# Kernel optimization log

Hardware: AMD Instinct MI355X
Metric: run time of the kernel (lower is better)

## Reference

```python
import jax, jax.numpy as jnp
import numpy as np

B, N, N2 = 4, 4096, 4096
CIN, DIM, KNN, UP = 128, 64, 20, 2
HPOS, HATT = 64, 256
EPS = 1e-5


def _group(feat, idx):
    # feat: (B,C,M), idx: (B,N,K) -> (B,C,N,K) gather of neighbor features
    return jax.vmap(lambda f, i: f[:, i])(feat, idx)


def _conv1d(w, b, x):
    # 1x1 Conv1d: w (O,C), x (B,C,N)
    return jnp.einsum('oc,bcn->bon', w, x) + b[:, None]


def _bn(x, g, be, m, v):
    # eval-mode BatchNorm2d on (B,C,N,K)
    inv = g / jnp.sqrt(v + EPS)
    return x * inv[:, None, None] + (be - m * inv)[:, None, None]


def setup_inputs() -> dict:
    key = jax.random.key(0)
    ks = jax.random.split(key, 32)
    r = lambda i, s: jax.random.normal(ks[i], s, jnp.float32)
    u = lambda i, s: jax.random.uniform(ks[i], s, jnp.float32, 0.5, 1.5)
    return {
        'pos1': r(0, (B, 3, N)),
        'query': r(1, (B, CIN, N)),
        'pos2': r(2, (B, 3, N2)),
        'key_feat': r(3, (B, CIN, N2)),
        'wq': r(4, (DIM, CIN)) * 0.05, 'bq': r(5, (DIM,)) * 0.05,
        'wk': r(6, (DIM, CIN)) * 0.05, 'bk': r(7, (DIM,)) * 0.05,
        'wv': r(8, (DIM, CIN)) * 0.05, 'bv': r(9, (DIM,)) * 0.05,
        'pw1': r(10, (HPOS, 3)) * 0.2, 'pb1': r(11, (HPOS,)) * 0.05,
        'pg': u(12, (HPOS,)), 'pbt': r(13, (HPOS,)) * 0.05,
        'pm': r(14, (HPOS,)) * 0.05, 'pv': u(15, (HPOS,)),
        'pw2': r(16, (DIM, HPOS)) * 0.1, 'pb2': r(17, (DIM,)) * 0.05,
        'aw1': r(18, (HATT, DIM)) * 0.1, 'ab1': r(19, (HATT,)) * 0.05,
        'ag': u(20, (HATT,)), 'abt2': r(21, (HATT,)) * 0.05,
        'am': r(22, (HATT,)) * 0.05, 'av': u(23, (HATT,)),
        'awt': r(24, (HATT, DIM, UP)) * 0.05, 'abt': r(25, (DIM,)) * 0.05,
        'we': r(26, (CIN, DIM)) * 0.1, 'be': r(27, (CIN,)) * 0.05,
    }


def reference(pos1, query, pos2, key_feat, wq, bq, wk, bk, wv, bv,
              pw1, pb1, pg, pbt, pm, pv, pw2, pb2,
              aw1, ab1, ag, abt2, am, av, awt, abt, we, be):
    q = _conv1d(wq, bq, query)          # (B,DIM,N)
    k = _conv1d(wk, bk, key_feat)       # (B,DIM,N2)
    v = _conv1d(wv, bv, key_feat)       # (B,DIM,N2)
    # KNN of pos1 queries into pos2 support set
    p1 = pos1.transpose(0, 2, 1)        # (B,N,3)
    p2 = pos2.transpose(0, 2, 1)        # (B,N2,3)
    d = (jnp.sum(p1 * p1, -1)[:, :, None] + jnp.sum(p2 * p2, -1)[:, None, :]
         - 2.0 * jnp.einsum('bnd,bmd->bnm', p1, p2))
    _, idx = jax.lax.top_k(-d, KNN)     # (B,N,KNN)
    kg = _group(k, idx)                 # (B,DIM,N,K)
    qk_rel = q[:, :, :, None] - kg
    pos_rel = pos1[:, :, :, None] - _group(pos2, idx)   # (B,3,N,K)
    # pos_mlp: conv2d 3->HPOS, BN, ReLU, conv2d HPOS->DIM
    pe = jnp.einsum('oc,bcnk->bonk', pw1, pos_rel) + pb1[:, None, None]
    pe = jax.nn.relu(_bn(pe, pg, pbt, pm, pv))
    pe = jnp.einsum('oc,bcnk->bonk', pw2, pe) + pb2[:, None, None]  # (B,DIM,N,K)
    # attn_mlp: conv2d DIM->HATT, BN, ReLU, ConvTranspose2d HATT->DIM kernel (UP,1)
    h = qk_rel + pe
    a = jnp.einsum('oc,bcnk->bonk', aw1, h) + ab1[:, None, None]
    a = jax.nn.relu(_bn(a, ag, abt2, am, av))               # (B,HATT,N,K)
    att = jnp.einsum('bcnk,cor->bonrk', a, awt).reshape(B, DIM, N * UP, KNN)
    att = att + abt[:, None, None]
    att = jax.nn.softmax(att, axis=-1)
    vg = _group(v, idx) + pe            # (B,DIM,N,K)
    vu = jnp.repeat(vg, UP, axis=2)     # nearest upsample -> (B,DIM,N*UP,K)
    agg = jnp.sum(att * vu, axis=-1)    # (B,DIM,N*UP)
    y = _conv1d(we, be, agg)            # (B,CIN,N*UP)
    identity = jnp.repeat(query, UP, axis=2)  # residual (in==out -> Identity)
    return y + identity
```

## Files before the change

kernel.cpp:

```cpp
#include <hip/hip_runtime.h>
#include <hip/hip_bf16.h>

#define BATCH 4
#define NPTS  4096
#define NPTS2 4096
#define CIN   128
#define DIM   64
#define KNN   20
#define UPF   2
#define HPOS  64
#define HATT  256
#define MOUT  8192
#define EPSF  1e-5f
#define QPB   3
#define BPB   1366

typedef _Float16 h16x8 __attribute__((ext_vector_type(8)));
typedef _Float16 h16x4 __attribute__((ext_vector_type(4)));
typedef _Float16 h16x2 __attribute__((ext_vector_type(2)));
typedef float    f32x4 __attribute__((ext_vector_type(4)));

__device__ inline float rdlane(float v, int src) {
  return __int_as_float(__builtin_amdgcn_readlane(__float_as_int(v), src));
}

__device__ __forceinline__ float distf(float qn, float m2x, float m2y, float m2z,
                                       float x, float y, float z) {
  float s = __fmaf_rn(x, x, qn);
  s = __fmaf_rn(y, y, s);
  s = __fmaf_rn(z, z, s);
  s = __fmaf_rn(m2x, x, s);
  s = __fmaf_rn(m2y, y, s);
  s = __fmaf_rn(m2z, z, s);
  return s;
}

__global__ __launch_bounds__(256) void proj_q(const float* __restrict__ x,
    const float* __restrict__ wq, const float* __restrict__ bq,
    float* __restrict__ q_t) {
  __shared__ float X[CIN][64];
  __shared__ float O[64][65];
  const int b  = blockIdx.x >> 6;
  const int n0 = (blockIdx.x & 63) * 64;
  const int t  = threadIdx.x;
  for (int l = t; l < CIN * 64; l += 256) {
    int c = l >> 6, i = l & 63;
    X[c][i] = x[(b * CIN + c) * NPTS + n0 + i];
  }
  __syncthreads();
  const int n_l = t & 63;
  const int w   = __builtin_amdgcn_readfirstlane(t >> 6);
  float acc[16];
#pragma unroll
  for (int i = 0; i < 16; ++i) acc[i] = bq[w * 16 + i];
  for (int c = 0; c < CIN; ++c) {
    float xv = X[c][n_l];
#pragma unroll
    for (int i = 0; i < 16; ++i) acc[i] += wq[(w * 16 + i) * CIN + c] * xv;
  }
#pragma unroll
  for (int i = 0; i < 16; ++i) O[n_l][w * 16 + i] = acc[i];
  __syncthreads();
  for (int l = t; l < 64 * 64; l += 256)
    q_t[(b * NPTS + n0 + (l >> 6)) * DIM + (l & 63)] = O[l >> 6][l & 63];
}

__global__ __launch_bounds__(256) void proj_kv(const float* __restrict__ x,
    const float* __restrict__ wk, const float* __restrict__ bk,
    const float* __restrict__ wv, const float* __restrict__ bv,
    float* __restrict__ k_t, float* __restrict__ v_t) {
  __shared__ float X[CIN][64];
  __shared__ float O[64][65];
  const int b  = blockIdx.x >> 6;
  const int n0 = (blockIdx.x & 63) * 64;
  const int t  = threadIdx.x;
  for (int l = t; l < CIN * 64; l += 256) {
    int c = l >> 6, i = l & 63;
    X[c][i] = x[(b * CIN + c) * NPTS2 + n0 + i];
  }
  __syncthreads();
  const int n_l = t & 63;
  const int w   = __builtin_amdgcn_readfirstlane(t >> 6);
  float acck[16], accv[16];
#pragma unroll
  for (int i = 0; i < 16; ++i) { acck[i] = bk[w * 16 + i]; accv[i] = bv[w * 16 + i]; }
  for (int c = 0; c < CIN; ++c) {
    float xv = X[c][n_l];
#pragma unroll
    for (int i = 0; i < 16; ++i) {
      acck[i] += wk[(w * 16 + i) * CIN + c] * xv;
      accv[i] += wv[(w * 16 + i) * CIN + c] * xv;
    }
  }
#pragma unroll
  for (int i = 0; i < 16; ++i) O[n_l][w * 16 + i] = acck[i];
  __syncthreads();
  for (int l = t; l < 64 * 64; l += 256)
    k_t[(b * NPTS2 + n0 + (l >> 6)) * DIM + (l & 63)] = O[l >> 6][l & 63];
  __syncthreads();
#pragma unroll
  for (int i = 0; i < 16; ++i) O[n_l][w * 16 + i] = accv[i];
  __syncthreads();
  for (int l = t; l < 64 * 64; l += 256)
    v_t[(b * NPTS2 + n0 + (l >> 6)) * DIM + (l & 63)] = O[l >> 6][l & 63];
}

__global__ __launch_bounds__(256) void knn_kernel(const float* __restrict__ pos1,
    const float* __restrict__ pos2, int* __restrict__ idxout) {
  __shared__ int   cntS[16];
  __shared__ float dbufS[16][64];
  __shared__ int   jbufS[16][64];
  const int lane = threadIdx.x & 63;
  const int wv   = threadIdx.x >> 6;
  const int b    = blockIdx.x >> 8;
  const int nb   = (blockIdx.x & 255) * 16;
  const float* p2x = pos2 + (b * 3 + 0) * NPTS2;
  const float* p2y = pos2 + (b * 3 + 1) * NPTS2;
  const float* p2z = pos2 + (b * 3 + 2) * NPTS2;

  float qn[4], m2x[4], m2y[4], m2z[4];
#pragma unroll
  for (int qi = 0; qi < 4; ++qi) {
    int n = nb + wv * 4 + qi;
    float qx = pos1[(b * 3 + 0) * NPTS + n];
    float qy = pos1[(b * 3 + 1) * NPTS + n];
    float qz = pos1[(b * 3 + 2) * NPTS + n];
    qn[qi]  = qx * qx + qy * qy + qz * qz;
    m2x[qi] = -2.0f * qx; m2y[qi] = -2.0f * qy; m2z[qi] = -2.0f * qz;
  }

  float mymin[4] = {3.402823466e38f, 3.402823466e38f,
                    3.402823466e38f, 3.402823466e38f};
  f32x4 cx[4], cy[4], cz[4];
#pragma unroll 1
  for (int c = 0; c < 4; ++c) {
    int base = c * 1024 + lane * 4;
#pragma unroll
    for (int g = 0; g < 4; ++g) {
      cx[g] = *(const f32x4*)(p2x + base + g * 256);
      cy[g] = *(const f32x4*)(p2y + base + g * 256);
      cz[g] = *(const f32x4*)(p2z + base + g * 256);
    }
#pragma unroll
    for (int qi = 0; qi < 4; ++qi)
#pragma unroll
      for (int g = 0; g < 4; ++g)
#pragma unroll
        for (int e = 0; e < 4; ++e) {
          float d = distf(qn[qi], m2x[qi], m2y[qi], m2z[qi],
                          cx[g][e], cy[g][e], cz[g][e]);
          mymin[qi] = fminf(mymin[qi], d);
        }
  }

  float T0[4];
#pragma unroll
  for (int qi = 0; qi < 4; ++qi) {
    float v = mymin[qi];
#pragma unroll
    for (int k = 2; k <= 64; k <<= 1)
#pragma unroll
      for (int jj = k >> 1; jj >= 1; jj >>= 1) {
        float o = __shfl_xor(v, jj);
        bool up = ((lane & k) == 0);
        bool keepmin = (((lane & jj) == 0) == up);
        v = keepmin ? fminf(v, o) : fmaxf(v, o);
      }
    T0[qi] = rdlane(v, 19);
  }

  if (lane < 4) cntS[wv * 4 + lane] = 0;

#pragma unroll 1
  for (int c = 0; c < 4; ++c) {
    int base = c * 1024 + lane * 4;
#pragma unroll
    for (int g = 0; g < 4; ++g) {
      cx[g] = *(const f32x4*)(p2x + base + g * 256);
      cy[g] = *(const f32x4*)(p2y + base + g * 256);
      cz[g] = *(const f32x4*)(p2z + base + g * 256);
    }
#pragma unroll
    for (int qi = 0; qi < 4; ++qi) {
      const int qq = wv * 4 + qi;
#pragma unroll
      for (int g = 0; g < 4; ++g)
#pragma unroll
        for (int e = 0; e < 4; ++e) {
          float d = distf(qn[qi], m2x[qi], m2y[qi], m2z[qi],
                          cx[g][e], cy[g][e], cz[g][e]);
          if (d <= T0[qi]) {
            int slot = atomicAdd(&cntS[qq], 1);
            if (slot < 64) { dbufS[qq][slot] = d; jbufS[qq][slot] = base + g * 256 + e; }
          }
        }
    }
  }

#pragma unroll 1
  for (int qi = 0; qi < 4; ++qi) {
    const int qq = wv * 4 + qi;
    const int n  = nb + qq;
    const int cnt = cntS[qq];
    if (cnt <= 64) {
      float dk = (lane < cnt) ? dbufS[qq][lane] : 3.402823466e38f;
      int   jk = (lane < cnt) ? jbufS[qq][lane] : 0x7fffffff;
#pragma unroll
      for (int k = 2; k <= 64; k <<= 1) {
#pragma unroll
        for (int jj = k >> 1; jj >= 1; jj >>= 1) {
          float od = __shfl_xor(dk, jj);
          int   oj = __shfl_xor(jk, jj);
          bool mineSm = (dk < od) || (dk == od && jk < oj);
          bool up = ((lane & k) == 0);
          bool keepmin = (((lane & jj) == 0) == up);
          bool takeOther = (keepmin != mineSm);
          dk = takeOther ? od : dk;
          jk = takeOther ? oj : jk;
        }
      }
      if (lane < KNN) idxout[(b * NPTS + n) * KNN + lane] = jk;
    } else {
      float dl = 3.402823466e38f;
      int   il = 0;
      for (int j0 = 0; j0 < NPTS2; j0 += 64) {
        int j = j0 + lane;
        float d = distf(qn[qi], m2x[qi], m2y[qi], m2z[qi], p2x[j], p2y[j], p2z[j]);
        float T = rdlane(dl, 19);
        unsigned long long m = __ballot(d < T);
        while (m) {
          int src = __ffsll(m) - 1;
          m &= m - 1;
          float dd = rdlane(d, src);
          float T2 = rdlane(dl, 19);
          if (dd < T2) {
            int jj2 = j0 + src;
            float pd = __shfl_up(dl, 1);
            int   pi = __shfl_up(il, 1);
            if (dl > dd) {
              if (lane == 0 || pd <= dd) { dl = dd; il = jj2; }
              else                       { dl = pd; il = pi; }
            }
          }
        }
      }
      if (lane < KNN) idxout[(b * NPTS + n) * KNN + lane] = il;
    }
  }
}

__global__ __launch_bounds__(256) void pack_weights(
    const float* __restrict__ aw1, const float* __restrict__ awt,
    const float* __restrict__ pw2,
    const float* __restrict__ ag,  const float* __restrict__ av,
    const float* __restrict__ abt2, const float* __restrict__ am,
    const float* __restrict__ abt,
    const float* __restrict__ pg,  const float* __restrict__ pv,
    const float* __restrict__ pbt, const float* __restrict__ pm,
    const float* __restrict__ ab1, const float* __restrict__ pb1,
    const float* __restrict__ pw1,
    _Float16* __restrict__ aw1h, _Float16* __restrict__ awtP,
    _Float16* __restrict__ pw2h, float* __restrict__ abtX,
    float* __restrict__ ab1f, float* __restrict__ pw1f,
    float* __restrict__ pb1f) {
  int i = blockIdx.x * 256 + threadIdx.x;
  if (i < 16384) {
    int j = i >> 6;
    float inv = ag[j] / sqrtf(av[j] + EPSF);
    aw1h[i] = (_Float16)(aw1[i] * inv);
  }
  if (i < 32768) {
    int orr = i >> 8, j = i & 255;
    awtP[i] = (_Float16)awt[j * 128 + orr];
  }
  if (i < 4096) pw2h[i] = (_Float16)pw2[i];
  if (i < 256) {
    float inv = ag[i] / sqrtf(av[i] + EPSF);
    ab1f[i] = ab1[i] * inv + (abt2[i] - am[i] * inv);
  }
  if (i < 192) {
    int hc = i / 3;
    float inv = pg[hc] / sqrtf(pv[hc] + EPSF);
    pw1f[i] = pw1[i] * inv;
  }
  if (i < 128) abtX[i] = abt[i >> 1];
  if (i < 64) {
    float inv = pg[i] / sqrtf(pv[i] + EPSF);
    pb1f[i] = pb1[i] * inv + (pbt[i] - pm[i] * inv);
  }
}

#define SM_R0    0
#define SM_R1    9216
#define SM_LGC   0
#define SM_VGB   18432

__global__ __launch_bounds__(256, 4) void attn_mfma(
    const float* __restrict__ q_t, const float* __restrict__ k_t,
    const float* __restrict__ v_t, const int* __restrict__ idx,
    const float* __restrict__ pos1, const float* __restrict__ pos2,
    const float* __restrict__ pw1f, const float* __restrict__ pb1f,
    const _Float16* __restrict__ pw2h, const float* __restrict__ pb2,
    const _Float16* __restrict__ aw1h, const float* __restrict__ ab1f,
    const _Float16* __restrict__ awtP, const float* __restrict__ abtX,
    float* __restrict__ agg) {
  __shared__ __align__(16) char smem[27136];
  const int b  = blockIdx.x / BPB;
  const int n0 = (blockIdx.x - b * BPB) * QPB;
  const int t  = threadIdx.x;
  const int lane = t & 63;
  const int w  = t >> 6;
  const int r  = lane & 15;
  const int q4 = lane >> 4;

  const int colB = t & 63, cgB = t >> 6;
  const int pB = colB / 20, kkB = colB - pB * 20;
  const bool okB = (pB < QPB) && (n0 + pB < NPTS);
  const int nqB = okB ? (n0 + pB) : 0;
  int jB = 0;
  if (okB) jB = idx[(b * NPTS + nqB) * KNN + kkB];

  f32x4 qk4[4], vv4[4];
  {
    const float* qrow = q_t + ((size_t)(b * NPTS  + nqB)) * DIM + cgB * 16;
    const float* krow = k_t + ((size_t)(b * NPTS2 + jB))  * DIM + cgB * 16;
    const float* vrow = v_t + ((size_t)(b * NPTS2 + jB))  * DIM + cgB * 16;
#pragma unroll
    for (int u = 0; u < 4; ++u) {
      f32x4 qv = *(const f32x4*)(qrow + u * 4);
      f32x4 kv = *(const f32x4*)(krow + u * 4);
      qk4[u] = qv - kv;
      vv4[u] = *(const f32x4*)(vrow + u * 4);
    }
  }

  {
    float p0 = 0.f, p1 = 0.f, p2 = 0.f;
    if (okB) {
      p0 = pos1[(b * 3 + 0) * NPTS + nqB] - pos2[(b * 3 + 0) * NPTS2 + jB];
      p1 = pos1[(b * 3 + 1) * NPTS + nqB] - pos2[(b * 3 + 1) * NPTS2 + jB];
      p2 = pos1[(b * 3 + 2) * NPTS + nqB] - pos2[(b * 3 + 2) * NPTS2 + jB];
    }
#pragma unroll
    for (int hf = 0; hf < 2; ++hf) {
      h16x8 pk;
#pragma unroll
      for (int ii = 0; ii < 8; ++ii) {
        int hc = cgB * 16 + hf * 8 + ii;
        float v0 = pb1f[hc] + pw1f[hc*3] * p0 + pw1f[hc*3+1] * p1 + pw1f[hc*3+2] * p2;
        v0 = fmaxf(v0, 0.f);
        if (!okB) v0 = 0.f;
        pk[ii] = (_Float16)v0;
      }
      *(h16x8*)(smem + SM_R0 + ((colB * 72 + cgB * 16 + hf * 8) * 2)) = pk;
    }
  }
  __syncthreads();

  {
    h16x8 a0[2];
#pragma unroll
    for (int ks = 0; ks < 2; ++ks)
      a0[ks] = *(const h16x8*)&pw2h[(w * 16 + r) * 64 + ks * 32 + q4 * 8];
    f32x4 acc[4];
#pragma unroll
    for (int nt = 0; nt < 4; ++nt) acc[nt] = (f32x4){0.f, 0.f, 0.f, 0.f};
#pragma unroll
    for (int ks = 0; ks < 2; ++ks)
#pragma unroll
      for (int nt = 0; nt < 4; ++nt) {
        h16x8 bv = *(h16x8*)(smem + SM_R0 + ((nt * 16 + r) * 72 + ks * 32 + q4 * 8) * 2);
        acc[nt] = __builtin_amdgcn_mfma_f32_16x16x32_f16(a0[ks], bv, acc[nt], 0, 0, 0);
      }
    int o0 = w * 16 + q4 * 4;
    f32x4 pbv = *(const f32x4*)&pb2[o0];
#pragma unroll
    for (int nt = 0; nt < 4; ++nt) {
      f32x4 vv = acc[nt] + pbv;
      h16x4 pk = {(_Float16)vv[0], (_Float16)vv[1], (_Float16)vv[2], (_Float16)vv[3]};
      *(h16x4*)(smem + SM_R1 + ((nt * 16 + r) * 72 + o0) * 2) = pk;
    }
  }

  {
    h16x8 pe8[2];
#pragma unroll
    for (int hf = 0; hf < 2; ++hf)
      pe8[hf] = *(h16x8*)(smem + SM_R1 + (colB * 72 + cgB * 16 + hf * 8) * 2);
    h16x8 hp8[2];
#pragma unroll
    for (int u = 0; u < 4; ++u) {
      int hf = u >> 1, e0 = (u & 1) * 4;
      f32x4 pe = {(float)pe8[hf][e0],     (float)pe8[hf][e0 + 1],
                  (float)pe8[hf][e0 + 2], (float)pe8[hf][e0 + 3]};
      f32x4 hv = qk4[u] + pe;
      f32x4 gv = vv4[u] + pe;
      if (!okB) { hv = (f32x4){0.f,0.f,0.f,0.f}; gv = hv; }
      hp8[hf][e0]     = (_Float16)hv[0];
      hp8[hf][e0 + 1] = (_Float16)hv[1];
      hp8[hf][e0 + 2] = (_Float16)hv[2];
      hp8[hf][e0 + 3] = (_Float16)hv[3];
      h16x4 gp = {(_Float16)gv[0], (_Float16)gv[1], (_Float16)gv[2], (_Float16)gv[3]};
      *(h16x4*)(smem + SM_VGB + (colB * 68 + cgB * 16 + u * 4) * 2) = gp;
    }
#pragma unroll
    for (int hf = 0; hf < 2; ++hf)
      *(h16x8*)(smem + SM_R1 + (colB * 72 + cgB * 16 + hf * 8) * 2) = hp8[hf];
  }
  __syncthreads();

  h16x8 bs[2][4];
#pragma unroll
  for (int ks = 0; ks < 2; ++ks)
#pragma unroll
    for (int nt = 0; nt < 4; ++nt)
      bs[ks][nt] = *(h16x8*)(smem + SM_R1 + ((nt * 16 + r) * 72 + ks * 32 + q4 * 8) * 2);

  f32x4 accD[2][4];
#pragma unroll
  for (int h = 0; h < 2; ++h)
#pragma unroll
    for (int nt = 0; nt < 4; ++nt) accD[h][nt] = (f32x4){0.f, 0.f, 0.f, 0.f};

#define C_QUARTER(quar, base)                                                  \
  {                                                                            \
    int mt = (quar) * 4 + w;                                                   \
    h16x8 af0 = *(const h16x8*)&aw1h[(mt * 16 + r) * 64 + q4 * 8];             \
    h16x8 af1 = *(const h16x8*)&aw1h[(mt * 16 + r) * 64 + 32 + q4 * 8];        \
    f32x4 acc[4];                                                              \
    _Pragma("unroll")                                                          \
    for (int nt = 0; nt < 4; ++nt) acc[nt] = (f32x4){0.f, 0.f, 0.f, 0.f};      \
    _Pragma("unroll")                                                          \
    for (int nt = 0; nt < 4; ++nt)                                             \
      acc[nt] = __builtin_amdgcn_mfma_f32_16x16x32_f16(af0, bs[0][nt], acc[nt], 0, 0, 0); \
    _Pragma("unroll")                                                          \
    for (int nt = 0; nt < 4; ++nt)                                             \
      acc[nt] = __builtin_amdgcn_mfma_f32_16x16x32_f16(af1, bs[1][nt], acc[nt], 0, 0, 0); \
    int j0  = mt * 16 + q4 * 4;                                                \
    int jq0 = j0 - (quar) * 64;                                                \
    f32x4 b1 = *(const f32x4*)&ab1f[j0];                                       \
    _Pragma("unroll")                                                          \
    for (int nt = 0; nt < 4; ++nt) {                                           \
      int col = nt * 16 + r;                                                   \
      float v0 = fmaxf(acc[nt][0] + b1[0], 0.f);                               \
      float v1 = fmaxf(acc[nt][1] + b1[1], 0.f);                               \
      float v2 = fmaxf(acc[nt][2] + b1[2], 0.f);                               \
      float v3 = fmaxf(acc[nt][3] + b1[3], 0.f);                               \
      h16x4 pk = {(_Float16)v0, (_Float16)v1, (_Float16)v2, (_Float16)v3};     \
      *(h16x4*)(smem + (base) + (col * 72 + jq0) * 2) = pk;                    \
    }                                                                          \
  }

#define D_QUARTER(quar, base)                                                  \
  {                                                                            \
    _Pragma("unroll")                                                          \
    for (int ks2 = 0; ks2 < 2; ++ks2) {                                        \
      h16x8 bsv[4];                                                            \
      _Pragma("unroll")                                                        \
      for (int nt = 0; nt < 4; ++nt)                                           \
        bsv[nt] = *(h16x8*)(smem + (base) + ((nt * 16 + r) * 72 + ks2 * 32 + q4 * 8) * 2); \
      int ksg = (quar) * 2 + ks2;                                              \
      _Pragma("unroll")                                                        \
      for (int h = 0; h < 2; ++h) {                                            \
        int mt2 = w * 2 + h;                                                   \
        h16x8 af = *(const h16x8*)&awtP[(mt2 * 16 + r) * 256 + ksg * 32 + q4 * 8]; \
        _Pragma("unroll")                                                      \
        for (int nt = 0; nt < 4; ++nt)                                         \
          accD[h][nt] = __builtin_amdgcn_mfma_f32_16x16x32_f16(af, bsv[nt], accD[h][nt], 0, 0, 0); \
      }                                                                        \
    }                                                                          \
  }

  C_QUARTER(0, SM_R0)
  __syncthreads();
  D_QUARTER(0, SM_R0)
  C_QUARTER(1, SM_R1)
  __syncthreads();
  D_QUARTER(1, SM_R1)
  C_QUARTER(2, SM_R0)
  __syncthreads();
  D_QUARTER(2, SM_R0)
  C_QUARTER(3, SM_R1)
  __syncthreads();
  D_QUARTER(3, SM_R1)
  __syncthreads();

  {
#pragma unroll
    for (int h = 0; h < 2; ++h) {
      int orr0 = (w * 2 + h) * 16 + q4 * 4;
      f32x4 ab = *(const f32x4*)&abtX[orr0];
#pragma unroll
      for (int nt = 0; nt < 4; ++nt) {
        int col = nt * 16 + r;
        if (col < QPB * KNN) {
          f32x4 vv = accD[h][nt] + ab;
          h16x4 pk = {(_Float16)vv[0], (_Float16)vv[1], (_Float16)vv[2], (_Float16)vv[3]};
          *(h16x4*)(smem + SM_LGC + (col * 136 + orr0) * 2) = pk;
        }
      }
    }
  }
  __syncthreads();

  if (t < 64 * QPB) {
    int li = t & 63, p = t >> 6;
    if (n0 + p < NPTS) {
      h16x2 Lp[KNN];
      float G[KNN];
#pragma unroll
      for (int kk = 0; kk < KNN; ++kk) {
        Lp[kk] = *(h16x2*)(smem + SM_LGC + ((p * 20 + kk) * 136 + li * 2) * 2);
        G[kk]  = (float)*(_Float16*)(smem + SM_VGB + ((p * 20 + kk) * 68 + li) * 2);
      }
#pragma unroll
      for (int half = 0; half < 2; ++half) {
        float mx = (float)Lp[0][half];
#pragma unroll
        for (int kk = 1; kk < KNN; ++kk) mx = fmaxf(mx, (float)Lp[kk][half]);
        float s = 0.f, a = 0.f;
#pragma unroll
        for (int kk = 0; kk < KNN; ++kk) {
          float e = __expf((float)Lp[kk][half] - mx);
          s += e;
          a += e * G[kk];
        }
        float rs = 1.0f / s;
        agg[(((size_t)(b * NPTS + n0 + p)) * UPF + half) * DIM + li] = a * rs;
      }
    }
  }
#undef C_QUARTER
#undef D_QUARTER
}

__global__ __launch_bounds__(256) void out_proj(const float* __restrict__ agg,
    const float* __restrict__ we, const float* __restrict__ be,
    const float* __restrict__ query, float* __restrict__ out) {
  __shared__ float A[64][65];
  const int b  = blockIdx.x >> 7;
  const int m0 = (blockIdx.x & 127) * 64;
  const int t  = threadIdx.x;
  for (int l = t; l < 64 * 64; l += 256) {
    int row = l >> 6, c = l & 63;
    A[row][c] = agg[(b * MOUT + m0 + row) * DIM + c];
  }
  __syncthreads();
  const int m_l = t & 63;
  const int w   = __builtin_amdgcn_readfirstlane(t >> 6);
  float acc[32];
#pragma unroll
  for (int i = 0; i < 32; ++i) acc[i] = 0.f;
  for (int c = 0; c < DIM; ++c) {
    float a = A[m_l][c];
#pragma unroll
    for (int i = 0; i < 32; ++i) acc[i] += we[(w * 32 + i) * DIM + c] * a;
  }
  const int m = m0 + m_l;
#pragma unroll
  for (int i = 0; i < 32; ++i) {
    int o = w * 32 + i;
    out[(b * CIN + o) * MOUT + m] = acc[i] + be[o] + query[(b * CIN + o) * NPTS + (m >> 1)];
  }
}

extern "C" void kernel_launch(void* const* d_in, const int* in_sizes, int n_in,
                              void* d_out, int out_size, void* d_ws, size_t ws_size,
                              hipStream_t stream) {
  (void)in_sizes; (void)n_in; (void)out_size; (void)ws_size;
  const float* pos1     = (const float*)d_in[0];
  const float* query    = (const float*)d_in[1];
  const float* pos2     = (const float*)d_in[2];
  const float* key_feat = (const float*)d_in[3];
  const float* wq  = (const float*)d_in[4];
  const float* bq  = (const float*)d_in[5];
  const float* wk  = (const float*)d_in[6];
  const float* bk  = (const float*)d_in[7];
  const float* wv  = (const float*)d_in[8];
  const float* bv  = (const float*)d_in[9];
  const float* pw1 = (const float*)d_in[10];
  const float* pb1 = (const float*)d_in[11];
  const float* pg  = (const float*)d_in[12];
  const float* pbt = (const float*)d_in[13];
  const float* pm  = (const float*)d_in[14];
  const float* pv  = (const float*)d_in[15];
  const float* pw2 = (const float*)d_in[16];
  const float* pb2 = (const float*)d_in[17];
  const float* aw1 = (const float*)d_in[18];
  const float* ab1 = (const float*)d_in[19];
  const float* ag  = (const float*)d_in[20];
  const float* abt2= (const float*)d_in[21];
  const float* am  = (const float*)d_in[22];
  const float* av  = (const float*)d_in[23];
  const float* awt = (const float*)d_in[24];
  const float* abt = (const float*)d_in[25];
  const float* we  = (const float*)d_in[26];
  const float* be  = (const float*)d_in[27];

  float* ws   = (float*)d_ws;
  float* q_t  = ws;
  float* k_t  = q_t + BATCH * NPTS * DIM;
  float* v_t  = k_t + BATCH * NPTS2 * DIM;
  float* aggb = v_t + BATCH * NPTS2 * DIM;
  int*   idxb = (int*)(aggb + BATCH * MOUT * DIM);
  _Float16* aw1h = (_Float16*)(idxb + BATCH * NPTS * KNN);
  _Float16* awtP = aw1h + HATT * DIM;
  _Float16* pw2h = awtP + 128 * HATT;
  float* abtX    = (float*)(pw2h + DIM * HPOS);
  float* ab1f    = abtX + 128;
  float* pw1f    = ab1f + HATT;
  float* pb1f    = pw1f + HPOS * 3;

  pack_weights<<<128, 256, 0, stream>>>(aw1, awt, pw2, ag, av, abt2, am, abt,
      pg, pv, pbt, pm, ab1, pb1, pw1,
      aw1h, awtP, pw2h, abtX, ab1f, pw1f, pb1f);
  proj_q <<<BATCH * (NPTS / 64), 256, 0, stream>>>(query, wq, bq, q_t);
  proj_kv<<<BATCH * (NPTS2 / 64), 256, 0, stream>>>(key_feat, wk, bk, wv, bv, k_t, v_t);
  knn_kernel<<<BATCH * NPTS / 16, 256, 0, stream>>>(pos1, pos2, idxb);
  attn_mfma<<<BATCH * BPB, 256, 0, stream>>>(q_t, k_t, v_t, idxb, pos1, pos2,
      pw1f, pb1f, pw2h, pb2, aw1h, ab1f, awtP, abtX, aggb);
  out_proj<<<BATCH * (MOUT / 64), 256, 0, stream>>>(aggb, we, be, query, (float*)d_out);
}
```

Measured before the change: 346.1 us.

## Merge KNN, projections and weight packing into one front kernel

Four independent prologue kernels (KNN, k/v projection, q projection, weight packing) are combined into one launch, with each role chosen by block-index range and shared memory held in a union. This removes three launch gaps and lets the independent stages run at the same time on the GPU instead of one after another. In exchange, the shared-memory footprint and register allocation now follow the largest branch, which may reduce occupancy for the lighter roles.

New measurement: 318.4 us. -8.0%, faster.

```diff
diff --git a/kernel.cpp b/kernel.cpp
--- a/kernel.cpp
+++ b/kernel.cpp
@@ -15,6 +15,11 @@
 #define QPB   3
 #define BPB   1366
 
+#define FB_KNN   1024
+#define FB_PKV   (FB_KNN + 256)
+#define FB_PQ    (FB_PKV + 256)
+#define FB_PACK  (FB_PQ + 128)
+
 typedef _Float16 h16x8 __attribute__((ext_vector_type(8)));
 typedef _Float16 h16x4 __attribute__((ext_vector_type(4)));
 typedef _Float16 h16x2 __attribute__((ext_vector_type(2)));
@@ -35,221 +40,16 @@
   return s;
 }
 
-__global__ __launch_bounds__(256) void proj_q(const float* __restrict__ x,
-    const float* __restrict__ wq, const float* __restrict__ bq,
-    float* __restrict__ q_t) {
-  __shared__ float X[CIN][64];
-  __shared__ float O[64][65];
-  const int b  = blockIdx.x >> 6;
-  const int n0 = (blockIdx.x & 63) * 64;
-  const int t  = threadIdx.x;
-  for (int l = t; l < CIN * 64; l += 256) {
-    int c = l >> 6, i = l & 63;
-    X[c][i] = x[(b * CIN + c) * NPTS + n0 + i];
-  }
-  __syncthreads();
-  const int n_l = t & 63;
-  const int w   = __builtin_amdgcn_readfirstlane(t >> 6);
-  float acc[16];
-#pragma unroll
-  for (int i = 0; i < 16; ++i) acc[i] = bq[w * 16 + i];
-  for (int c = 0; c < CIN; ++c) {
-    float xv = X[c][n_l];
-#pragma unroll
-    for (int i = 0; i < 16; ++i) acc[i] += wq[(w * 16 + i) * CIN + c] * xv;
-  }
-#pragma unroll
-  for (int i = 0; i < 16; ++i) O[n_l][w * 16 + i] = acc[i];
-  __syncthreads();
-  for (int l = t; l < 64 * 64; l += 256)
-    q_t[(b * NPTS + n0 + (l >> 6)) * DIM + (l & 63)] = O[l >> 6][l & 63];
-}
-
-__global__ __launch_bounds__(256) void proj_kv(const float* __restrict__ x,
+__global__ __launch_bounds__(256) void front(
+    const float* __restrict__ pos1, const float* __restrict__ pos2,
+    int* __restrict__ idxout,
+    const float* __restrict__ key_feat,
     const float* __restrict__ wk, const float* __restrict__ bk,
     const float* __restrict__ wv, const float* __restrict__ bv,
-    float* __restrict__ k_t, float* __restrict__ v_t) {
-  __shared__ float X[CIN][64];
-  __shared__ float O[64][65];
-  const int b  = blockIdx.x >> 6;
-  const int n0 = (blockIdx.x & 63) * 64;
-  const int t  = threadIdx.x;
-  for (int l = t; l < CIN * 64; l += 256) {
-    int c = l >> 6, i = l & 63;
-    X[c][i] = x[(b * CIN + c) * NPTS2 + n0 + i];
-  }
-  __syncthreads();
-  const int n_l = t & 63;
-  const int w   = __builtin_amdgcn_readfirstlane(t >> 6);
-  float acck[16], accv[16];
-#pragma unroll
-  for (int i = 0; i < 16; ++i) { acck[i] = bk[w * 16 + i]; accv[i] = bv[w * 16 + i]; }
-  for (int c = 0; c < CIN; ++c) {
-    float xv = X[c][n_l];
-#pragma unroll
-    for (int i = 0; i < 16; ++i) {
-      acck[i] += wk[(w * 16 + i) * CIN + c] * xv;
-      accv[i] += wv[(w * 16 + i) * CIN + c] * xv;
-    }
-  }
-#pragma unroll
-  for (int i = 0; i < 16; ++i) O[n_l][w * 16 + i] = acck[i];
-  __syncthreads();
-  for (int l = t; l < 64 * 64; l += 256)
-    k_t[(b * NPTS2 + n0 + (l >> 6)) * DIM + (l & 63)] = O[l >> 6][l & 63];
-  __syncthreads();
-#pragma unroll
-  for (int i = 0; i < 16; ++i) O[n_l][w * 16 + i] = accv[i];
-  __syncthreads();
-  for (int l = t; l < 64 * 64; l += 256)
-    v_t[(b * NPTS2 + n0 + (l >> 6)) * DIM + (l & 63)] = O[l >> 6][l & 63];
-}
-
-__global__ __launch_bounds__(256) void knn_kernel(const float* __restrict__ pos1,
-    const float* __restrict__ pos2, int* __restrict__ idxout) {
-  __shared__ int   cntS[16];
-  __shared__ float dbufS[16][64];
-  __shared__ int   jbufS[16][64];
-  const int lane = threadIdx.x & 63;
-  const int wv   = threadIdx.x >> 6;
-  const int b    = blockIdx.x >> 8;
-  const int nb   = (blockIdx.x & 255) * 16;
-  const float* p2x = pos2 + (b * 3 + 0) * NPTS2;
-  const float* p2y = pos2 + (b * 3 + 1) * NPTS2;
-  const float* p2z = pos2 + (b * 3 + 2) * NPTS2;
-
-  float qn[4], m2x[4], m2y[4], m2z[4];
-#pragma unroll
-  for (int qi = 0; qi < 4; ++qi) {
-    int n = nb + wv * 4 + qi;
-    float qx = pos1[(b * 3 + 0) * NPTS + n];
-    float qy = pos1[(b * 3 + 1) * NPTS + n];
-    float qz = pos1[(b * 3 + 2) * NPTS + n];
-    qn[qi]  = qx * qx + qy * qy + qz * qz;
-    m2x[qi] = -2.0f * qx; m2y[qi] = -2.0f * qy; m2z[qi] = -2.0f * qz;
-  }
-
-  float mymin[4] = {3.402823466e38f, 3.402823466e38f,
-                    3.402823466e38f, 3.402823466e38f};
-  f32x4 cx[4], cy[4], cz[4];
-#pragma unroll 1
-  for (int c = 0; c < 4; ++c) {
-    int base = c * 1024 + lane * 4;
-#pragma unroll
-    for (int g = 0; g < 4; ++g) {
-      cx[g] = *(const f32x4*)(p2x + base + g * 256);
-      cy[g] = *(const f32x4*)(p2y + base + g * 256);
-      cz[g] = *(const f32x4*)(p2z + base + g * 256);
-    }
-#pragma unroll
-    for (int qi = 0; qi < 4; ++qi)
-#pragma unroll
-      for (int g = 0; g < 4; ++g)
-#pragma unroll
-        for (int e = 0; e < 4; ++e) {
-          float d = distf(qn[qi], m2x[qi], m2y[qi], m2z[qi],
-                          cx[g][e], cy[g][e], cz[g][e]);
-          mymin[qi] = fminf(mymin[qi], d);
-        }
-  }
-
-  float T0[4];
-#pragma unroll
-  for (int qi = 0; qi < 4; ++qi) {
-    float v = mymin[qi];
-#pragma unroll
-    for (int k = 2; k <= 64; k <<= 1)
-#pragma unroll
-      for (int jj = k >> 1; jj >= 1; jj >>= 1) {
-        float o = __shfl_xor(v, jj);
-        bool up = ((lane & k) == 0);
-        bool keepmin = (((lane & jj) == 0) == up);
-        v = keepmin ? fminf(v, o) : fmaxf(v, o);
-      }
-    T0[qi] = rdlane(v, 19);
-  }
-
-  if (lane < 4) cntS[wv * 4 + lane] = 0;
-
-#pragma unroll 1
-  for (int c = 0; c < 4; ++c) {
-    int base = c * 1024 + lane * 4;
-#pragma unroll
-    for (int g = 0; g < 4; ++g) {
-      cx[g] = *(const f32x4*)(p2x + base + g * 256);
-      cy[g] = *(const f32x4*)(p2y + base + g * 256);
-      cz[g] = *(const f32x4*)(p2z + base + g * 256);
-    }
-#pragma unroll
-    for (int qi = 0; qi < 4; ++qi) {
-      const int qq = wv * 4 + qi;
-#pragma unroll
-      for (int g = 0; g < 4; ++g)
-#pragma unroll
-        for (int e = 0; e < 4; ++e) {
-          float d = distf(qn[qi], m2x[qi], m2y[qi], m2z[qi],
-                          cx[g][e], cy[g][e], cz[g][e]);
-          if (d <= T0[qi]) {
-            int slot = atomicAdd(&cntS[qq], 1);
-            if (slot < 64) { dbufS[qq][slot] = d; jbufS[qq][slot] = base + g * 256 + e; }
-          }
-        }
-    }
-  }
-
-#pragma unroll 1
-  for (int qi = 0; qi < 4; ++qi) {
-    const int qq = wv * 4 + qi;
-    const int n  = nb + qq;
-    const int cnt = cntS[qq];
-    if (cnt <= 64) {
-      float dk = (lane < cnt) ? dbufS[qq][lane] : 3.402823466e38f;
-      int   jk = (lane < cnt) ? jbufS[qq][lane] : 0x7fffffff;
-#pragma unroll
-      for (int k = 2; k <= 64; k <<= 1) {
-#pragma unroll
-        for (int jj = k >> 1; jj >= 1; jj >>= 1) {
-          float od = __shfl_xor(dk, jj);
-          int   oj = __shfl_xor(jk, jj);
-          bool mineSm = (dk < od) || (dk == od && jk < oj);
-          bool up = ((lane & k) == 0);
-          bool keepmin = (((lane & jj) == 0) == up);
-          bool takeOther = (keepmin != mineSm);
-          dk = takeOther ? od : dk;
-          jk = takeOther ? oj : jk;
-        }
-      }
-      if (lane < KNN) idxout[(b * NPTS + n) * KNN + lane] = jk;
-    } else {
-      float dl = 3.402823466e38f;
-      int   il = 0;
-      for (int j0 = 0; j0 < NPTS2; j0 += 64) {
-        int j = j0 + lane;
-        float d = distf(qn[qi], m2x[qi], m2y[qi], m2z[qi], p2x[j], p2y[j], p2z[j]);
-        float T = rdlane(dl, 19);
-        unsigned long long m = __ballot(d < T);
-        while (m) {
-          int src = __ffsll(m) - 1;
-          m &= m - 1;
-          float dd = rdlane(d, src);
-          float T2 = rdlane(dl, 19);
-          if (dd < T2) {
-            int jj2 = j0 + src;
-            float pd = __shfl_up(dl, 1);
-            int   pi = __shfl_up(il, 1);
-            if (dl > dd) {
-              if (lane == 0 || pd <= dd) { dl = dd; il = jj2; }
-              else                       { dl = pd; il = pi; }
-            }
-          }
-        }
-      }
-      if (lane < KNN) idxout[(b * NPTS + n) * KNN + lane] = il;
-    }
-  }
-}
-
-__global__ __launch_bounds__(256) void pack_weights(
+    float* __restrict__ k_t, float* __restrict__ v_t,
+    const float* __restrict__ query,
+    const float* __restrict__ wq, const float* __restrict__ bq,
+    float* __restrict__ q_t,
     const float* __restrict__ aw1, const float* __restrict__ awt,
     const float* __restrict__ pw2,
     const float* __restrict__ ag,  const float* __restrict__ av,
@@ -263,30 +63,234 @@
     _Float16* __restrict__ pw2h, float* __restrict__ abtX,
     float* __restrict__ ab1f, float* __restrict__ pw1f,
     float* __restrict__ pb1f) {
-  int i = blockIdx.x * 256 + threadIdx.x;
-  if (i < 16384) {
-    int j = i >> 6;
-    float inv = ag[j] / sqrtf(av[j] + EPSF);
-    aw1h[i] = (_Float16)(aw1[i] * inv);
-  }
-  if (i < 32768) {
-    int orr = i >> 8, j = i & 255;
-    awtP[i] = (_Float16)awt[j * 128 + orr];
-  }
-  if (i < 4096) pw2h[i] = (_Float16)pw2[i];
-  if (i < 256) {
-    float inv = ag[i] / sqrtf(av[i] + EPSF);
-    ab1f[i] = ab1[i] * inv + (abt2[i] - am[i] * inv);
-  }
-  if (i < 192) {
-    int hc = i / 3;
-    float inv = pg[hc] / sqrtf(pv[hc] + EPSF);
-    pw1f[i] = pw1[i] * inv;
-  }
-  if (i < 128) abtX[i] = abt[i >> 1];
-  if (i < 64) {
-    float inv = pg[i] / sqrtf(pv[i] + EPSF);
-    pb1f[i] = pb1[i] * inv + (pbt[i] - pm[i] * inv);
+  __shared__ union {
+    struct { float X[CIN][64]; float O[64][65]; } pj;
+    struct { int cnt[16]; float dbuf[16][64]; int jbuf[16][64]; } kn;
+  } smU;
+  const int bid = blockIdx.x;
+  const int t   = threadIdx.x;
+
+  if (bid < FB_KNN) {
+    const int lane = t & 63;
+    const int wv   = t >> 6;
+    const int b    = bid >> 8;
+    const int nb   = (bid & 255) * 16;
+    const float* p2x = pos2 + (b * 3 + 0) * NPTS2;
+    const float* p2y = pos2 + (b * 3 + 1) * NPTS2;
+    const float* p2z = pos2 + (b * 3 + 2) * NPTS2;
+
+    float qn[4], m2x[4], m2y[4], m2z[4];
+#pragma unroll
+    for (int qi = 0; qi < 4; ++qi) {
+      int n = nb + wv * 4 + qi;
+      float qx = pos1[(b * 3 + 0) * NPTS + n];
+      float qy = pos1[(b * 3 + 1) * NPTS + n];
+      float qz = pos1[(b * 3 + 2) * NPTS + n];
+      qn[qi]  = qx * qx + qy * qy + qz * qz;
+      m2x[qi] = -2.0f * qx; m2y[qi] = -2.0f * qy; m2z[qi] = -2.0f * qz;
+    }
+
+    float mymin[4] = {3.402823466e38f, 3.402823466e38f,
+                      3.402823466e38f, 3.402823466e38f};
+    f32x4 cx[4], cy[4], cz[4];
+#pragma unroll 1
+    for (int c = 0; c < 4; ++c) {
+      int base = c * 1024 + lane * 4;
+#pragma unroll
+      for (int g = 0; g < 4; ++g) {
+        cx[g] = *(const f32x4*)(p2x + base + g * 256);
+        cy[g] = *(const f32x4*)(p2y + base + g * 256);
+        cz[g] = *(const f32x4*)(p2z + base + g * 256);
+      }
+#pragma unroll
+      for (int qi = 0; qi < 4; ++qi)
+#pragma unroll
+        for (int g = 0; g < 4; ++g)
+#pragma unroll
+          for (int e = 0; e < 4; ++e) {
+            float d = distf(qn[qi], m2x[qi], m2y[qi], m2z[qi],
+                            cx[g][e], cy[g][e], cz[g][e]);
+            mymin[qi] = fminf(mymin[qi], d);
+          }
+    }
+
+    float T0[4];
+#pragma unroll
+    for (int qi = 0; qi < 4; ++qi) {
+      float v = mymin[qi];
+#pragma unroll
+      for (int k = 2; k <= 64; k <<= 1)
+#pragma unroll
+        for (int jj = k >> 1; jj >= 1; jj >>= 1) {
+          float o = __shfl_xor(v, jj);
+          bool up = ((lane & k) == 0);
+          bool keepmin = (((lane & jj) == 0) == up);
+          v = keepmin ? fminf(v, o) : fmaxf(v, o);
+        }
+      T0[qi] = rdlane(v, 19);
+    }
+
+    if (lane < 4) smU.kn.cnt[wv * 4 + lane] = 0;
+
+#pragma unroll 1
+    for (int c = 0; c < 4; ++c) {
+      int base = c * 1024 + lane * 4;
+#pragma unroll
+      for (int g = 0; g < 4; ++g) {
+        cx[g] = *(const f32x4*)(p2x + base + g * 256);
+        cy[g] = *(const f32x4*)(p2y + base + g * 256);
+        cz[g] = *(const f32x4*)(p2z + base + g * 256);
+      }
+#pragma unroll
+      for (int qi = 0; qi < 4; ++qi) {
+        const int qq = wv * 4 + qi;
+#pragma unroll
+        for (int g = 0; g < 4; ++g)
+#pragma unroll
+          for (int e = 0; e < 4; ++e) {
+            float d = distf(qn[qi], m2x[qi], m2y[qi], m2z[qi],
+                            cx[g][e], cy[g][e], cz[g][e]);
+            if (d <= T0[qi]) {
+              int slot = atomicAdd(&smU.kn.cnt[qq], 1);
+              if (slot < 64) { smU.kn.dbuf[qq][slot] = d; smU.kn.jbuf[qq][slot] = base + g * 256 + e; }
+            }
+          }
+      }
+    }
+
+#pragma unroll 1
+    for (int qi = 0; qi < 4; ++qi) {
+      const int qq = wv * 4 + qi;
+      const int n  = nb + qq;
+      const int cnt = smU.kn.cnt[qq];
+      if (cnt <= 64) {
+        float dk = (lane < cnt) ? smU.kn.dbuf[qq][lane] : 3.402823466e38f;
+        int   jk = (lane < cnt) ? smU.kn.jbuf[qq][lane] : 0x7fffffff;
+#pragma unroll
+        for (int k = 2; k <= 64; k <<= 1) {
+#pragma unroll
+          for (int jj = k >> 1; jj >= 1; jj >>= 1) {
+            float od = __shfl_xor(dk, jj);
+            int   oj = __shfl_xor(jk, jj);
+            bool mineSm = (dk < od) || (dk == od && jk < oj);
+            bool up = ((lane & k) == 0);
+            bool keepmin = (((lane & jj) == 0) == up);
+            bool takeOther = (keepmin != mineSm);
+            dk = takeOther ? od : dk;
+            jk = takeOther ? oj : jk;
+          }
+        }
+        if (lane < KNN) idxout[(b * NPTS + n) * KNN + lane] = jk;
+      } else {
+        float dl = 3.402823466e38f;
+        int   il = 0;
+        for (int j0 = 0; j0 < NPTS2; j0 += 64) {
+          int j = j0 + lane;
+          float d = distf(qn[qi], m2x[qi], m2y[qi], m2z[qi], p2x[j], p2y[j], p2z[j]);
+          float T = rdlane(dl, 19);
+          unsigned long long m = __ballot(d < T);
+          while (m) {
+            int src = __ffsll(m) - 1;
+            m &= m - 1;
+            float dd = rdlane(d, src);
+            float T2 = rdlane(dl, 19);
+            if (dd < T2) {
+              int jj2 = j0 + src;
+              float pd = __shfl_up(dl, 1);
+              int   pi = __shfl_up(il, 1);
+              if (dl > dd) {
+                if (lane == 0 || pd <= dd) { dl = dd; il = jj2; }
+                else                       { dl = pd; il = pi; }
+              }
+            }
+          }
+        }
+        if (lane < KNN) idxout[(b * NPTS + n) * KNN + lane] = il;
+      }
+    }
+  } else if (bid < FB_PKV) {
+    const int vb = bid - FB_KNN;
+    const int b  = vb >> 6;
+    const int n0 = (vb & 63) * 64;
+    for (int l = t; l < CIN * 64; l += 256) {
+      int c = l >> 6, i = l & 63;
+      smU.pj.X[c][i] = key_feat[(b * CIN + c) * NPTS2 + n0 + i];
+    }
+    __syncthreads();
+    const int n_l = t & 63;
+    const int w   = __builtin_amdgcn_readfirstlane(t >> 6);
+    float acck[16], accv[16];
+#pragma unroll
+    for (int i = 0; i < 16; ++i) { acck[i] = bk[w * 16 + i]; accv[i] = bv[w * 16 + i]; }
+    for (int c = 0; c < CIN; ++c) {
+      float xv = smU.pj.X[c][n_l];
+#pragma unroll
+      for (int i = 0; i < 16; ++i) {
+        acck[i] += wk[(w * 16 + i) * CIN + c] * xv;
+        accv[i] += wv[(w * 16 + i) * CIN + c] * xv;
+      }
+    }
+#pragma unroll
+    for (int i = 0; i < 16; ++i) smU.pj.O[n_l][w * 16 + i] = acck[i];
+    __syncthreads();
+    for (int l = t; l < 64 * 64; l += 256)
+      k_t[(b * NPTS2 + n0 + (l >> 6)) * DIM + (l & 63)] = smU.pj.O[l >> 6][l & 63];
+    __syncthreads();
+#pragma unroll
+    for (int i = 0; i < 16; ++i) smU.pj.O[n_l][w * 16 + i] = accv[i];
+    __syncthreads();
+    for (int l = t; l < 64 * 64; l += 256)
+      v_t[(b * NPTS2 + n0 + (l >> 6)) * DIM + (l & 63)] = smU.pj.O[l >> 6][l & 63];
+  } else if (bid < FB_PQ) {
+    const int vb = bid - FB_PKV;
+    const int b  = vb >> 6;
+    const int n0 = (vb & 63) * 64;
+    for (int l = t; l < CIN * 64; l += 256) {
+      int c = l >> 6, i = l & 63;
+      smU.pj.X[c][i] = query[(b * CIN + c) * NPTS + n0 + i];
+    }
+    __syncthreads();
+    const int n_l = t & 63;
+    const int w   = __builtin_amdgcn_readfirstlane(t >> 6);
+    float acc[16];
+#pragma unroll
+    for (int i = 0; i < 16; ++i) acc[i] = bq[w * 16 + i];
+    for (int c = 0; c < CIN; ++c) {
+      float xv = smU.pj.X[c][n_l];
+#pragma unroll
+      for (int i = 0; i < 16; ++i) acc[i] += wq[(w * 16 + i) * CIN + c] * xv;
+    }
+#pragma unroll
+    for (int i = 0; i < 16; ++i) smU.pj.O[n_l][w * 16 + i] = acc[i];
+    __syncthreads();
+    for (int l = t; l < 64 * 64; l += 256)
+      q_t[(b * NPTS + n0 + (l >> 6)) * DIM + (l & 63)] = smU.pj.O[l >> 6][l & 63];
+  } else {
+    int i = (bid - FB_PQ) * 256 + t;
+    if (i < 16384) {
+      int j = i >> 6;
+      float inv = ag[j] / sqrtf(av[j] + EPSF);
+      aw1h[i] = (_Float16)(aw1[i] * inv);
+    }
+    if (i < 32768) {
+      int orr = i >> 8, j = i & 255;
+      awtP[i] = (_Float16)awt[j * 128 + orr];
+    }
+    if (i < 4096) pw2h[i] = (_Float16)pw2[i];
+    if (i < 256) {
+      float inv = ag[i] / sqrtf(av[i] + EPSF);
+      ab1f[i] = ab1[i] * inv + (abt2[i] - am[i] * inv);
+    }
+    if (i < 192) {
+      int hc = i / 3;
+      float inv = pg[hc] / sqrtf(pv[hc] + EPSF);
+      pw1f[i] = pw1[i] * inv;
+    }
+    if (i < 128) abtX[i] = abt[i >> 1];
+    if (i < 64) {
+      float inv = pg[i] / sqrtf(pv[i] + EPSF);
+      pb1f[i] = pb1[i] * inv + (pbt[i] - pm[i] * inv);
+    }
   }
 }
 
@@ -611,12 +615,13 @@
   float* pw1f    = ab1f + HATT;
   float* pb1f    = pw1f + HPOS * 3;
 
-  pack_weights<<<128, 256, 0, stream>>>(aw1, awt, pw2, ag, av, abt2, am, abt,
+  front<<<FB_PACK, 256, 0, stream>>>(
+      pos1, pos2, idxb,
+      key_feat, wk, bk, wv, bv, k_t, v_t,
+      query, wq, bq, q_t,
+      aw1, awt, pw2, ag, av, abt2, am, abt,
       pg, pv, pbt, pm, ab1, pb1, pw1,
       aw1h, awtP, pw2h, abtX, ab1f, pw1f, pb1f);
-  proj_q <<<BATCH * (NPTS / 64), 256, 0, stream>>>(query, wq, bq, q_t);
-  proj_kv<<<BATCH * (NPTS2 / 64), 256, 0, stream>>>(key_feat, wk, bk, wv, bv, k_t, v_t);
-  knn_kernel<<<BATCH * NPTS / 16, 256, 0, stream>>>(pos1, pos2, idxb);
   attn_mfma<<<BATCH * BPB, 256, 0, stream>>>(q_t, k_t, v_t, idxb, pos1, pos2,
       pw1f, pb1f, pw2h, pb2, aw1h, ab1f, awtP, abtX, aggb);
   out_proj<<<BATCH * (MOUT / 64), 256, 0, stream>>>(aggb, we, be, query, (float*)d_out);
```
